# Performance work log

Hardware: AMD Instinct MI355X
Metric: run time of the kernel (lower is better)

Reference implementation:

```python
import jax, jax.numpy as jnp
import numpy as np

N_NODES = 100000
N_EDGES = 1600000
N_FEAT = 128
HIDDEN = 128
N_CLASSES = 10
N_GRAPHS = 512


def setup_inputs() -> dict:
    key = jax.random.key(0)
    ks = jax.random.split(key, 20)

    def lin(k, fan_in, fan_out, bias=True):
        kw, kb = jax.random.split(k)
        s = 1.0 / np.sqrt(fan_in)
        W = jax.random.uniform(kw, (fan_in, fan_out), jnp.float32, -s, s)
        if bias:
            b = jax.random.uniform(kb, (fan_out,), jnp.float32, -s, s)
            return W, b
        return W

    x = jax.random.normal(ks[0], (N_NODES, N_FEAT), jnp.float32)
    edge_index = jax.random.randint(ks[1], (2, N_EDGES), 0, N_NODES)
    batch = jnp.sort(jax.random.randint(ks[2], (N_NODES,), 0, N_GRAPHS))

    w1l, b1 = lin(ks[3], N_FEAT, HIDDEN)
    w1r = lin(ks[4], N_FEAT, HIDDEN, bias=False)
    w2l, b2 = lin(ks[5], HIDDEN, HIDDEN)
    w2r = lin(ks[6], HIDDEN, HIDDEN, bias=False)
    w3l, b3 = lin(ks[7], HIDDEN, HIDDEN)
    w3r = lin(ks[8], HIDDEN, HIDDEN, bias=False)
    gate_w, gate_b = lin(ks[9], HIDDEN, 1)
    lin1_w, lin1_b = lin(ks[10], HIDDEN, HIDDEN)
    lin2_w, lin2_b = lin(ks[11], HIDDEN, N_CLASSES)

    return dict(x=x, edge_index=edge_index, batch=batch,
                w1l=w1l, b1=b1, w1r=w1r,
                w2l=w2l, b2=b2, w2r=w2r,
                w3l=w3l, b3=b3, w3r=w3r,
                gate_w=gate_w, gate_b=gate_b,
                lin1_w=lin1_w, lin1_b=lin1_b,
                lin2_w=lin2_w, lin2_b=lin2_b)


def _sage_conv(x, src, dst, Wl, bl, Wr, n_nodes):
    # PyG SAGEConv(mean): out = lin_l(mean_{j in N(i)} x_j) + lin_r(x_i)
    msg_sum = jax.ops.segment_sum(x[src], dst, num_segments=n_nodes)
    cnt = jax.ops.segment_sum(jnp.ones((src.shape[0], 1), x.dtype), dst,
                              num_segments=n_nodes)
    mean = msg_sum / jnp.maximum(cnt, 1.0)
    return mean @ Wl + bl + x @ Wr


def reference(x, edge_index, batch,
              w1l, b1, w1r, w2l, b2, w2r, w3l, b3, w3r,
              gate_w, gate_b, lin1_w, lin1_b, lin2_w, lin2_b):
    n = x.shape[0]
    src, dst = edge_index[0], edge_index[1]

    h = jax.nn.relu(_sage_conv(x, src, dst, w1l, b1, w1r, n))
    h = jax.nn.relu(_sage_conv(h, src, dst, w2l, b2, w2r, n))
    h = jax.nn.relu(_sage_conv(h, src, dst, w3l, b3, w3r, n))

    # AttentionalAggregation: scatter-softmax of gate over graph segments
    gate = h @ gate_w + gate_b                                  # [N, 1]
    m = jax.ops.segment_max(gate, batch, num_segments=N_GRAPHS)  # [G, 1]
    e = jnp.exp(gate - m[batch])
    s = jax.ops.segment_sum(e, batch, num_segments=N_GRAPHS)     # [G, 1]
    alpha = e / s[batch]
    pooled = jax.ops.segment_sum(alpha * h, batch, num_segments=N_GRAPHS)  # [G, H]

    out = jax.nn.relu(pooled @ lin1_w + lin1_b)
    # dropout is identity in eval mode
    out = out @ lin2_w + lin2_b
    return jax.nn.log_softmax(out, axis=-1)
```

## Files before the change

### kernel.cpp

```cpp
#include <hip/hip_runtime.h>
#include <stdint.h>

#define N_NODES 100000
#define N_EDGES 1600000
#define NF 128
#define NG 512
#define NC 10

#define NBUCK ((N_NODES + 255) / 256)
#define EPB 8192

#define BSTRIDE 264

#define CVT_B 6250
#define BT_B 384
#define BOUNDS_B 3
#define COUNT_B ((N_EDGES + EPB - 1) / EPB)

typedef short short8 __attribute__((ext_vector_type(8)));
typedef float f32x4 __attribute__((ext_vector_type(4)));

__device__ __forceinline__ unsigned short f2b(float f) {
    unsigned u = __float_as_uint(f);
    u += 0x7fffu + ((u >> 16) & 1u);
    return (unsigned short)(u >> 16);
}
__device__ __forceinline__ float lo16(unsigned v) { return __uint_as_float(v << 16); }
__device__ __forceinline__ float hi16(unsigned v) { return __uint_as_float(v & 0xffff0000u); }

__global__ __launch_bounds__(256) void prep_kernel(const float* __restrict__ x, unsigned short* __restrict__ xb,
                                                   const float* __restrict__ w1l, const float* __restrict__ w1r,
                                                   const float* __restrict__ w2l, const float* __restrict__ w2r,
                                                   const float* __restrict__ w3l, const float* __restrict__ w3r,
                                                   unsigned short* __restrict__ Bt,
                                                   const int* __restrict__ batch, int* __restrict__ gstart,
                                                   const int* __restrict__ dst, int* __restrict__ bcount) {
    const int b = blockIdx.x, t = threadIdx.x;
    if (b < CVT_B) {
        int i = b * 256 + t;
        const float4* ip = (const float4*)x;
        float4 a = ip[2 * i], c = ip[2 * i + 1];
        uint4 o;
        o.x = (unsigned)f2b(a.x) | ((unsigned)f2b(a.y) << 16);
        o.y = (unsigned)f2b(a.z) | ((unsigned)f2b(a.w) << 16);
        o.z = (unsigned)f2b(c.x) | ((unsigned)f2b(c.y) << 16);
        o.w = (unsigned)f2b(c.z) | ((unsigned)f2b(c.w) << 16);
        ((uint4*)xb)[i] = o;
    } else if (b < CVT_B + BT_B) {
        int i = (b - CVT_B) * 256 + t;
        int layer = i / (128 * 256);
        int r = i % (128 * 256);
        int n = r / 256, k = r % 256;
        const float* wl = (layer == 0) ? w1l : (layer == 1) ? w2l : w3l;
        const float* wr = (layer == 0) ? w1r : (layer == 1) ? w2r : w3r;
        float v = (k < 128) ? wl[k * 128 + n] : wr[(k - 128) * 128 + n];
        Bt[i] = f2b(v);
    } else if (b < CVT_B + BT_B + BOUNDS_B) {
        int g = (b - CVT_B - BT_B) * 256 + t;
        if (g > NG) return;
        int lo = 0, hi = N_NODES;
        while (lo < hi) {
            int mid = (lo + hi) >> 1;
            if (batch[mid] < g) lo = mid + 1; else hi = mid;
        }
        gstart[g] = lo;
    } else {
        __shared__ int h[NBUCK];
        for (int i = t; i < NBUCK; i += 256) h[i] = 0;
        __syncthreads();
        const int base = (b - CVT_B - BT_B - BOUNDS_B) * EPB;
        const int lim = min(base + EPB, N_EDGES);
        for (int i = base + t; i < lim; i += 256) atomicAdd(&h[dst[i] >> 8], 1);
        __syncthreads();
        for (int i = t; i < NBUCK; i += 256)
            if (h[i]) atomicAdd(&bcount[i], h[i]);
    }
}

__global__ __launch_bounds__(512) void bucket_scan(const int* __restrict__ bcount, int* __restrict__ bbase,
                                                   int* __restrict__ gcursor, int* __restrict__ rowptr) {
    __shared__ int sh[512];
    const int t = threadIdx.x;
    int v = (t < NBUCK) ? bcount[t] : 0;
    sh[t] = v;
    __syncthreads();
    for (int off = 1; off < 512; off <<= 1) {
        int u = (t >= off) ? sh[t - off] : 0;
        __syncthreads();
        sh[t] += u;
        __syncthreads();
    }
    if (t < NBUCK) {
        int e = sh[t] - v;
        bbase[t] = e;
        gcursor[t] = e;
    }
    if (t == NBUCK - 1) bbase[NBUCK] = sh[t];
    if (t == 0) rowptr[N_NODES] = N_EDGES;
}

__global__ __launch_bounds__(256) void bucket_scatter(const int* __restrict__ src, const int* __restrict__ dst,
                                                      int* __restrict__ gcursor, unsigned* __restrict__ brec) {
    __shared__ int h[NBUCK];
    for (int i = threadIdx.x; i < NBUCK; i += 256) h[i] = 0;
    __syncthreads();
    const int base = blockIdx.x * EPB;
    const int lim = min(base + EPB, N_EDGES);
    for (int i = base + threadIdx.x; i < lim; i += 256) atomicAdd(&h[dst[i] >> 8], 1);
    __syncthreads();
    for (int i = threadIdx.x; i < NBUCK; i += 256) {
        int c = h[i];
        if (c) h[i] = atomicAdd(&gcursor[i], c);
    }
    __syncthreads();
    for (int i = base + threadIdx.x; i < lim; i += 256) {
        int d = dst[i];
        int pos = atomicAdd(&h[d >> 8], 1);
        brec[pos] = ((unsigned)(d & 255) << 17) | (unsigned)src[i];
    }
}

__global__ __launch_bounds__(256) void bucket_fill(const unsigned* __restrict__ brec, const int* __restrict__ bbase,
                                                   int* __restrict__ rowptr, int* __restrict__ eidx) {
    __shared__ int nh[256];
    __shared__ int sc[256];
    const int b = blockIdx.x, t = threadIdx.x;
    const int beg = bbase[b], end = bbase[b + 1];
    nh[t] = 0;
    __syncthreads();
    for (int i = beg + t; i < end; i += 256) atomicAdd(&nh[brec[i] >> 17], 1);
    __syncthreads();
    int cnt = nh[t];
    sc[t] = cnt;
    __syncthreads();
    for (int off = 1; off < 256; off <<= 1) {
        int u = (t >= off) ? sc[t - off] : 0;
        __syncthreads();
        sc[t] += u;
        __syncthreads();
    }
    int excl = sc[t] - cnt;
    int node = b * 256 + t;
    if (node < N_NODES) rowptr[node] = beg + excl;
    nh[t] = beg + excl;
    __syncthreads();
    for (int i = beg + t; i < end; i += 256) {
        unsigned r = brec[i];
        int pos = atomicAdd(&nh[r >> 17], 1);
        eidx[pos] = (int)(r & 0x1FFFFu);
    }
}

__global__ __launch_bounds__(256) void agg_kernel(const unsigned short* __restrict__ F,
                                                  const int* __restrict__ rowptr,
                                                  const int* __restrict__ eidx,
                                                  unsigned short* __restrict__ M) {
    int node = blockIdx.x * 4 + (threadIdx.x >> 6);
    if (node >= N_NODES) return;
    const int lane = threadIdx.x & 63;
    const int quad = lane >> 4, ql = lane & 15;
    const int beg = rowptr[node], end = rowptr[node + 1];
    const uint4* F4 = (const uint4*)F;

    float a0 = 0.f, a1 = 0.f, a2 = 0.f, a3 = 0.f, a4 = 0.f, a5 = 0.f, a6 = 0.f, a7 = 0.f;
    int t = beg + quad;
    for (; t + 12 < end; t += 16) {
        int r0 = eidx[t];
        int r1 = eidx[t + 4];
        int r2 = eidx[t + 8];
        int r3 = eidx[t + 12];
        uint4 v0 = F4[(size_t)r0 * 16 + ql];
        uint4 v1 = F4[(size_t)r1 * 16 + ql];
        uint4 v2 = F4[(size_t)r2 * 16 + ql];
        uint4 v3 = F4[(size_t)r3 * 16 + ql];
        a0 += lo16(v0.x) + lo16(v1.x) + lo16(v2.x) + lo16(v3.x);
        a1 += hi16(v0.x) + hi16(v1.x) + hi16(v2.x) + hi16(v3.x);
        a2 += lo16(v0.y) + lo16(v1.y) + lo16(v2.y) + lo16(v3.y);
        a3 += hi16(v0.y) + hi16(v1.y) + hi16(v2.y) + hi16(v3.y);
        a4 += lo16(v0.z) + lo16(v1.z) + lo16(v2.z) + lo16(v3.z);
        a5 += hi16(v0.z) + hi16(v1.z) + hi16(v2.z) + hi16(v3.z);
        a6 += lo16(v0.w) + lo16(v1.w) + lo16(v2.w) + lo16(v3.w);
        a7 += hi16(v0.w) + hi16(v1.w) + hi16(v2.w) + hi16(v3.w);
    }
    for (; t < end; t += 4) {
        uint4 v0 = F4[(size_t)eidx[t] * 16 + ql];
        a0 += lo16(v0.x); a1 += hi16(v0.x);
        a2 += lo16(v0.y); a3 += hi16(v0.y);
        a4 += lo16(v0.z); a5 += hi16(v0.z);
        a6 += lo16(v0.w); a7 += hi16(v0.w);
    }
    a0 += __shfl_xor(a0, 16); a0 += __shfl_xor(a0, 32);
    a1 += __shfl_xor(a1, 16); a1 += __shfl_xor(a1, 32);
    a2 += __shfl_xor(a2, 16); a2 += __shfl_xor(a2, 32);
    a3 += __shfl_xor(a3, 16); a3 += __shfl_xor(a3, 32);
    a4 += __shfl_xor(a4, 16); a4 += __shfl_xor(a4, 32);
    a5 += __shfl_xor(a5, 16); a5 += __shfl_xor(a5, 32);
    a6 += __shfl_xor(a6, 16); a6 += __shfl_xor(a6, 32);
    a7 += __shfl_xor(a7, 16); a7 += __shfl_xor(a7, 32);

    if (quad == 0) {
        float inv = 1.0f / (float)max(end - beg, 1);
        uint4 o;
        o.x = (unsigned)f2b(a0 * inv) | ((unsigned)f2b(a1 * inv) << 16);
        o.y = (unsigned)f2b(a2 * inv) | ((unsigned)f2b(a3 * inv) << 16);
        o.z = (unsigned)f2b(a4 * inv) | ((unsigned)f2b(a5 * inv) << 16);
        o.w = (unsigned)f2b(a6 * inv) | ((unsigned)f2b(a7 * inv) << 16);
        ((uint4*)M)[(size_t)node * 16 + ql] = o;
    }
}

__global__ __launch_bounds__(256, 2) void gemm_kernel(const unsigned short* __restrict__ Am,
                                                      const unsigned short* __restrict__ Ax,
                                                      const unsigned short* __restrict__ Bt,
                                                      const float* __restrict__ bias,
                                                      unsigned short* __restrict__ Out,
                                                      const float* __restrict__ gatew,
                                                      const float* __restrict__ gateb,
                                                      float* __restrict__ gate) {
    const int t = threadIdx.x;
    const int wave = t >> 6, lane = t & 63;
    const int lrow = lane & 15, quad = lane >> 4;
    const int row0 = blockIdx.x * 256 + wave * 64;

    __shared__ __attribute__((aligned(16))) unsigned short Bs[128 * BSTRIDE];

#pragma unroll
    for (int i = 0; i < 16; ++i) {
        int u = t + i * 256;
        int r = u >> 5, seg = u & 31;
        *(uint4*)(Bs + r * BSTRIDE + seg * 8) = *(const uint4*)(Bt + r * 256 + seg * 8);
    }
    __syncthreads();

    f32x4 acc[4][8];
#pragma unroll
    for (int i = 0; i < 4; ++i)
#pragma unroll
        for (int j = 0; j < 8; ++j) acc[i][j] = (f32x4){0.f, 0.f, 0.f, 0.f};

#pragma unroll
    for (int c = 0; c < 8; ++c) {
        const unsigned short* Aarr = (c < 4) ? Am : Ax;
        const int kb = (c & 3) * 32 + quad * 8;
        const int kf = c * 32 + quad * 8;
        short8 af[4];
#pragma unroll
        for (int i = 0; i < 4; ++i) {
            int ar = row0 + i * 16 + lrow;
            if (ar > N_NODES - 1) ar = N_NODES - 1;
            af[i] = *(const short8*)(Aarr + (size_t)ar * 128 + kb);
        }
#pragma unroll
        for (int j = 0; j < 8; ++j) {
            short8 bf = *(const short8*)(Bs + (j * 16 + lrow) * BSTRIDE + kf);
#pragma unroll
            for (int i = 0; i < 4; ++i)
                acc[i][j] = __builtin_amdgcn_mfma_f32_16x16x32_bf16(af[i], bf, acc[i][j], 0, 0, 0);
        }
    }

    float gpart[4][4];
#pragma unroll
    for (int i = 0; i < 4; ++i)
#pragma unroll
        for (int r = 0; r < 4; ++r) gpart[i][r] = 0.f;

#pragma unroll
    for (int j = 0; j < 8; ++j) {
        int col = j * 16 + lrow;
        float bc = bias[col];
        float gw = gatew ? gatew[col] : 0.f;
#pragma unroll
        for (int i = 0; i < 4; ++i) {
            int rbase = row0 + i * 16 + quad * 4;
#pragma unroll
            for (int r = 0; r < 4; ++r) {
                int row = rbase + r;
                if (row < N_NODES) {
                    float v = fmaxf(acc[i][j][r] + bc, 0.f);
                    Out[(size_t)row * 128 + col] = f2b(v);
                    gpart[i][r] += v * gw;
                }
            }
        }
    }
    if (gatew) {
        float gb = gateb[0];
#pragma unroll
        for (int i = 0; i < 4; ++i) {
#pragma unroll
            for (int r = 0; r < 4; ++r) {
                float g = gpart[i][r];
                g += __shfl_xor(g, 1);
                g += __shfl_xor(g, 2);
                g += __shfl_xor(g, 4);
                g += __shfl_xor(g, 8);
                if (lrow == 0) {
                    int row = row0 + i * 16 + quad * 4 + r;
                    if (row < N_NODES) gate[row] = g + gb;
                }
            }
        }
    }
}

__global__ __launch_bounds__(256) void pool_mlp_kernel(const unsigned short* __restrict__ h,
                                                       const float* __restrict__ gate,
                                                       const int* __restrict__ gstart,
                                                       const float* __restrict__ l1w,
                                                       const float* __restrict__ l1b,
                                                       const float* __restrict__ l2w,
                                                       const float* __restrict__ l2b,
                                                       float* __restrict__ out) {
    int wv = threadIdx.x >> 6;
    int g = blockIdx.x * 4 + wv;
    int lane = threadIdx.x & 63;
    __shared__ float pooled_s[4][128];
    __shared__ float hid_s[4][128];
    if (g >= NG) return;

    int beg = gstart[g], end = gstart[g + 1];

    float m = -INFINITY;
    for (int i = beg + lane; i < end; i += 64) m = fmaxf(m, gate[i]);
#pragma unroll
    for (int o = 32; o; o >>= 1) m = fmaxf(m, __shfl_xor(m, o));
    float s = 0.f;
    for (int i = beg + lane; i < end; i += 64) s += expf(gate[i] - m);
#pragma unroll
    for (int o = 32; o; o >>= 1) s += __shfl_xor(s, o);
    float invs = (s > 0.f) ? 1.0f / s : 0.f;

    float ax = 0.f, ay = 0.f;
    const unsigned* hb = (const unsigned*)h;
    int i = beg;
    for (; i + 2 <= end; i += 2) {
        float w0 = expf(gate[i] - m) * invs;
        float w1 = expf(gate[i + 1] - m) * invs;
        unsigned v0 = hb[(size_t)i * 64 + lane];
        unsigned v1 = hb[(size_t)(i + 1) * 64 + lane];
        ax += w0 * lo16(v0) + w1 * lo16(v1);
        ay += w0 * hi16(v0) + w1 * hi16(v1);
    }
    for (; i < end; ++i) {
        float w = expf(gate[i] - m) * invs;
        unsigned v = hb[(size_t)i * 64 + lane];
        ax += w * lo16(v);
        ay += w * hi16(v);
    }
    pooled_s[wv][2 * lane] = ax;
    pooled_s[wv][2 * lane + 1] = ay;

    float h0 = l1b[lane], h1 = l1b[lane + 64];
    for (int k = 0; k < 128; ++k) {
        float pv = pooled_s[wv][k];
        h0 += pv * l1w[k * 128 + lane];
        h1 += pv * l1w[k * 128 + lane + 64];
    }
    hid_s[wv][lane] = fmaxf(h0, 0.f);
    hid_s[wv][lane + 64] = fmaxf(h1, 0.f);

    float o10 = 0.f;
    if (lane < NC) {
        o10 = l2b[lane];
        for (int k = 0; k < 128; ++k) o10 += hid_s[wv][k] * l2w[k * NC + lane];
    }
    float mm = -INFINITY;
#pragma unroll
    for (int j = 0; j < NC; ++j) mm = fmaxf(mm, __shfl(o10, j));
    float ss = 0.f;
#pragma unroll
    for (int j = 0; j < NC; ++j) ss += expf(__shfl(o10, j) - mm);
    float lse = mm + logf(ss);
    if (lane < NC) out[g * NC + lane] = o10 - lse;
}

extern "C" void kernel_launch(void* const* d_in, const int* in_sizes, int n_in,
                              void* d_out, int out_size, void* d_ws, size_t ws_size,
                              hipStream_t stream) {
    const float* x   = (const float*)d_in[0];
    const int* ei    = (const int*)d_in[1];
    const int* batch = (const int*)d_in[2];
    const float* w1l = (const float*)d_in[3];
    const float* b1  = (const float*)d_in[4];
    const float* w1r = (const float*)d_in[5];
    const float* w2l = (const float*)d_in[6];
    const float* b2  = (const float*)d_in[7];
    const float* w2r = (const float*)d_in[8];
    const float* w3l = (const float*)d_in[9];
    const float* b3  = (const float*)d_in[10];
    const float* w3r = (const float*)d_in[11];
    const float* gw  = (const float*)d_in[12];
    const float* gb  = (const float*)d_in[13];
    const float* l1w = (const float*)d_in[14];
    const float* l1b = (const float*)d_in[15];
    const float* l2w = (const float*)d_in[16];
    const float* l2b = (const float*)d_in[17];
    float* out = (float*)d_out;

    const int* src = ei;
    const int* dst = ei + N_EDGES;

    char* base = (char*)d_ws;
    size_t off = 0;
    auto carve = [&](size_t bytes) -> void* {
        void* r = base + off;
        off = (off + bytes + 255) & ~(size_t)255;
        return r;
    };
    int* rowptr         = (int*)carve((size_t)(N_NODES + 1) * 4);
    int* eidx           = (int*)carve((size_t)N_EDGES * 4);
    unsigned short* Bt  = (unsigned short*)carve((size_t)3 * 128 * 256 * 2);
    unsigned short* xb  = (unsigned short*)carve((size_t)N_NODES * NF * 2);
    unsigned short* mn  = (unsigned short*)carve((size_t)N_NODES * NF * 2);
    unsigned short* hA  = (unsigned short*)carve((size_t)N_NODES * NF * 2);
    unsigned short* hB  = (unsigned short*)carve((size_t)N_NODES * NF * 2);
    float* gate         = (float*)carve((size_t)N_NODES * 4);
    int* gstart         = (int*)carve(513 * 4);
    int* bcount         = (int*)carve((NBUCK + 1) * 4);
    int* bbase          = (int*)carve((NBUCK + 1) * 4);
    int* gcursor        = (int*)carve((NBUCK + 1) * 4);
    unsigned* brec      = (unsigned*)mn;

    hipMemsetAsync(bcount, 0, (size_t)NBUCK * 4, stream);

    prep_kernel<<<CVT_B + BT_B + BOUNDS_B + COUNT_B, 256, 0, stream>>>(
        x, xb, w1l, w1r, w2l, w2r, w3l, w3r, Bt, batch, gstart, dst, bcount);

    bucket_scan<<<1, 512, 0, stream>>>(bcount, bbase, gcursor, rowptr);
    bucket_scatter<<<COUNT_B, 256, 0, stream>>>(src, dst, gcursor, brec);
    bucket_fill<<<NBUCK, 256, 0, stream>>>(brec, bbase, rowptr, eidx);

    const int AGG_B = (N_NODES + 3) / 4;
    const int GEMM_B = (N_NODES + 255) / 256;

    agg_kernel<<<AGG_B, 256, 0, stream>>>(xb, rowptr, eidx, mn);
    gemm_kernel<<<GEMM_B, 256, 0, stream>>>(mn, xb, Bt, b1, hA, nullptr, nullptr, nullptr);
    agg_kernel<<<AGG_B, 256, 0, stream>>>(hA, rowptr, eidx, mn);
    gemm_kernel<<<GEMM_B, 256, 0, stream>>>(mn, hA, Bt + 32768, b2, hB, nullptr, nullptr, nullptr);
    agg_kernel<<<AGG_B, 256, 0, stream>>>(hB, rowptr, eidx, mn);
    gemm_kernel<<<GEMM_B, 256, 0, stream>>>(mn, hB, Bt + 65536, b3, hA, gw, gb, gate);

    pool_mlp_kernel<<<(NG + 3) / 4, 256, 0, stream>>>(hA, gate, gstart, l1w, l1b, l2w, l2b, out);
}
```

Baseline: 507.0 us.

## Fuse neighbor-mean aggregation with MFMA GEMM per 64-node tile

Replaces the separate aggregation and GEMM kernels with one kernel per layer. Each block gathers neighbor means for 64 nodes into shared memory, then runs the bf16 MFMA GEMM in two 64-column passes with half-size weight tiles in LDS. This removes the global write and re-read of the mean buffer and three kernel launches. In exchange, each block reloads the weight tiles for only 64 rows and the gather phase is serialized with the GEMM inside a block, which may cut overlap and occupancy.

```diff
diff --git a/kernel.cpp b/kernel.cpp
--- a/kernel.cpp
+++ b/kernel.cpp
@@ -11,6 +11,7 @@
 #define EPB 8192
 
 #define BSTRIDE 264
+#define MSTRIDE 136
 
 #define CVT_B 6250
 #define BT_B 384
@@ -151,154 +152,144 @@
     }
 }
 
-__global__ __launch_bounds__(256) void agg_kernel(const unsigned short* __restrict__ F,
-                                                  const int* __restrict__ rowptr,
-                                                  const int* __restrict__ eidx,
-                                                  unsigned short* __restrict__ M) {
-    int node = blockIdx.x * 4 + (threadIdx.x >> 6);
-    if (node >= N_NODES) return;
-    const int lane = threadIdx.x & 63;
-    const int quad = lane >> 4, ql = lane & 15;
-    const int beg = rowptr[node], end = rowptr[node + 1];
-    const uint4* F4 = (const uint4*)F;
-
-    float a0 = 0.f, a1 = 0.f, a2 = 0.f, a3 = 0.f, a4 = 0.f, a5 = 0.f, a6 = 0.f, a7 = 0.f;
-    int t = beg + quad;
-    for (; t + 12 < end; t += 16) {
-        int r0 = eidx[t];
-        int r1 = eidx[t + 4];
-        int r2 = eidx[t + 8];
-        int r3 = eidx[t + 12];
-        uint4 v0 = F4[(size_t)r0 * 16 + ql];
-        uint4 v1 = F4[(size_t)r1 * 16 + ql];
-        uint4 v2 = F4[(size_t)r2 * 16 + ql];
-        uint4 v3 = F4[(size_t)r3 * 16 + ql];
-        a0 += lo16(v0.x) + lo16(v1.x) + lo16(v2.x) + lo16(v3.x);
-        a1 += hi16(v0.x) + hi16(v1.x) + hi16(v2.x) + hi16(v3.x);
-        a2 += lo16(v0.y) + lo16(v1.y) + lo16(v2.y) + lo16(v3.y);
-        a3 += hi16(v0.y) + hi16(v1.y) + hi16(v2.y) + hi16(v3.y);
-        a4 += lo16(v0.z) + lo16(v1.z) + lo16(v2.z) + lo16(v3.z);
-        a5 += hi16(v0.z) + hi16(v1.z) + hi16(v2.z) + hi16(v3.z);
-        a6 += lo16(v0.w) + lo16(v1.w) + lo16(v2.w) + lo16(v3.w);
-        a7 += hi16(v0.w) + hi16(v1.w) + hi16(v2.w) + hi16(v3.w);
-    }
-    for (; t < end; t += 4) {
-        uint4 v0 = F4[(size_t)eidx[t] * 16 + ql];
-        a0 += lo16(v0.x); a1 += hi16(v0.x);
-        a2 += lo16(v0.y); a3 += hi16(v0.y);
-        a4 += lo16(v0.z); a5 += hi16(v0.z);
-        a6 += lo16(v0.w); a7 += hi16(v0.w);
-    }
-    a0 += __shfl_xor(a0, 16); a0 += __shfl_xor(a0, 32);
-    a1 += __shfl_xor(a1, 16); a1 += __shfl_xor(a1, 32);
-    a2 += __shfl_xor(a2, 16); a2 += __shfl_xor(a2, 32);
-    a3 += __shfl_xor(a3, 16); a3 += __shfl_xor(a3, 32);
-    a4 += __shfl_xor(a4, 16); a4 += __shfl_xor(a4, 32);
-    a5 += __shfl_xor(a5, 16); a5 += __shfl_xor(a5, 32);
-    a6 += __shfl_xor(a6, 16); a6 += __shfl_xor(a6, 32);
-    a7 += __shfl_xor(a7, 16); a7 += __shfl_xor(a7, 32);
-
-    if (quad == 0) {
-        float inv = 1.0f / (float)max(end - beg, 1);
-        uint4 o;
-        o.x = (unsigned)f2b(a0 * inv) | ((unsigned)f2b(a1 * inv) << 16);
-        o.y = (unsigned)f2b(a2 * inv) | ((unsigned)f2b(a3 * inv) << 16);
-        o.z = (unsigned)f2b(a4 * inv) | ((unsigned)f2b(a5 * inv) << 16);
-        o.w = (unsigned)f2b(a6 * inv) | ((unsigned)f2b(a7 * inv) << 16);
-        ((uint4*)M)[(size_t)node * 16 + ql] = o;
-    }
-}
-
-__global__ __launch_bounds__(256, 2) void gemm_kernel(const unsigned short* __restrict__ Am,
-                                                      const unsigned short* __restrict__ Ax,
-                                                      const unsigned short* __restrict__ Bt,
-                                                      const float* __restrict__ bias,
-                                                      unsigned short* __restrict__ Out,
-                                                      const float* __restrict__ gatew,
-                                                      const float* __restrict__ gateb,
-                                                      float* __restrict__ gate) {
+__global__ __launch_bounds__(256) void fused_layer(const unsigned short* __restrict__ F,
+                                                   const int* __restrict__ rowptr,
+                                                   const int* __restrict__ eidx,
+                                                   const unsigned short* __restrict__ Bt,
+                                                   const float* __restrict__ bias,
+                                                   unsigned short* __restrict__ Out,
+                                                   const float* __restrict__ gatew,
+                                                   const float* __restrict__ gateb,
+                                                   float* __restrict__ gate) {
     const int t = threadIdx.x;
     const int wave = t >> 6, lane = t & 63;
     const int lrow = lane & 15, quad = lane >> 4;
-    const int row0 = blockIdx.x * 256 + wave * 64;
-
-    __shared__ __attribute__((aligned(16))) unsigned short Bs[128 * BSTRIDE];
-
-#pragma unroll
-    for (int i = 0; i < 16; ++i) {
-        int u = t + i * 256;
-        int r = u >> 5, seg = u & 31;
-        *(uint4*)(Bs + r * BSTRIDE + seg * 8) = *(const uint4*)(Bt + r * 256 + seg * 8);
-    }
-    __syncthreads();
-
-    f32x4 acc[4][8];
-#pragma unroll
-    for (int i = 0; i < 4; ++i)
-#pragma unroll
-        for (int j = 0; j < 8; ++j) acc[i][j] = (f32x4){0.f, 0.f, 0.f, 0.f};
-
-#pragma unroll
-    for (int c = 0; c < 8; ++c) {
-        const unsigned short* Aarr = (c < 4) ? Am : Ax;
-        const int kb = (c & 3) * 32 + quad * 8;
-        const int kf = c * 32 + quad * 8;
-        short8 af[4];
-#pragma unroll
-        for (int i = 0; i < 4; ++i) {
-            int ar = row0 + i * 16 + lrow;
-            if (ar > N_NODES - 1) ar = N_NODES - 1;
-            af[i] = *(const short8*)(Aarr + (size_t)ar * 128 + kb);
-        }
-#pragma unroll
-        for (int j = 0; j < 8; ++j) {
-            short8 bf = *(const short8*)(Bs + (j * 16 + lrow) * BSTRIDE + kf);
-#pragma unroll
-            for (int i = 0; i < 4; ++i)
-                acc[i][j] = __builtin_amdgcn_mfma_f32_16x16x32_bf16(af[i], bf, acc[i][j], 0, 0, 0);
-        }
-    }
-
-    float gpart[4][4];
-#pragma unroll
-    for (int i = 0; i < 4; ++i)
-#pragma unroll
-        for (int r = 0; r < 4; ++r) gpart[i][r] = 0.f;
-
-#pragma unroll
-    for (int j = 0; j < 8; ++j) {
-        int col = j * 16 + lrow;
-        float bc = bias[col];
-        float gw = gatew ? gatew[col] : 0.f;
-#pragma unroll
-        for (int i = 0; i < 4; ++i) {
-            int rbase = row0 + i * 16 + quad * 4;
+    const int row0 = blockIdx.x * 64;
+
+    __shared__ __attribute__((aligned(16))) unsigned short meanS[64 * MSTRIDE];
+    __shared__ __attribute__((aligned(16))) unsigned short Bs[64 * BSTRIDE];
+
+    const uint4* F4 = (const uint4*)F;
+
+    for (int n = 0; n < 16; ++n) {
+        int node = row0 + wave * 16 + n;
+        if (node >= N_NODES) break;
+        const int beg = rowptr[node], end = rowptr[node + 1];
+        float a0 = 0.f, a1 = 0.f, a2 = 0.f, a3 = 0.f, a4 = 0.f, a5 = 0.f, a6 = 0.f, a7 = 0.f;
+        int e = beg + quad;
+        for (; e + 12 < end; e += 16) {
+            int r0 = eidx[e];
+            int r1 = eidx[e + 4];
+            int r2 = eidx[e + 8];
+            int r3 = eidx[e + 12];
+            uint4 v0 = F4[(size_t)r0 * 16 + lrow];
+            uint4 v1 = F4[(size_t)r1 * 16 + lrow];
+            uint4 v2 = F4[(size_t)r2 * 16 + lrow];
+            uint4 v3 = F4[(size_t)r3 * 16 + lrow];
+            a0 += lo16(v0.x) + lo16(v1.x) + lo16(v2.x) + lo16(v3.x);
+            a1 += hi16(v0.x) + hi16(v1.x) + hi16(v2.x) + hi16(v3.x);
+            a2 += lo16(v0.y) + lo16(v1.y) + lo16(v2.y) + lo16(v3.y);
+            a3 += hi16(v0.y) + hi16(v1.y) + hi16(v2.y) + hi16(v3.y);
+            a4 += lo16(v0.z) + lo16(v1.z) + lo16(v2.z) + lo16(v3.z);
+            a5 += hi16(v0.z) + hi16(v1.z) + hi16(v2.z) + hi16(v3.z);
+            a6 += lo16(v0.w) + lo16(v1.w) + lo16(v2.w) + lo16(v3.w);
+            a7 += hi16(v0.w) + hi16(v1.w) + hi16(v2.w) + hi16(v3.w);
+        }
+        for (; e < end; e += 4) {
+            uint4 v0 = F4[(size_t)eidx[e] * 16 + lrow];
+            a0 += lo16(v0.x); a1 += hi16(v0.x);
+            a2 += lo16(v0.y); a3 += hi16(v0.y);
+            a4 += lo16(v0.z); a5 += hi16(v0.z);
+            a6 += lo16(v0.w); a7 += hi16(v0.w);
+        }
+        a0 += __shfl_xor(a0, 16); a0 += __shfl_xor(a0, 32);
+        a1 += __shfl_xor(a1, 16); a1 += __shfl_xor(a1, 32);
+        a2 += __shfl_xor(a2, 16); a2 += __shfl_xor(a2, 32);
+        a3 += __shfl_xor(a3, 16); a3 += __shfl_xor(a3, 32);
+        a4 += __shfl_xor(a4, 16); a4 += __shfl_xor(a4, 32);
+        a5 += __shfl_xor(a5, 16); a5 += __shfl_xor(a5, 32);
+        a6 += __shfl_xor(a6, 16); a6 += __shfl_xor(a6, 32);
+        a7 += __shfl_xor(a7, 16); a7 += __shfl_xor(a7, 32);
+        if (quad == 0) {
+            float inv = 1.0f / (float)max(end - beg, 1);
+            uint4 o;
+            o.x = (unsigned)f2b(a0 * inv) | ((unsigned)f2b(a1 * inv) << 16);
+            o.y = (unsigned)f2b(a2 * inv) | ((unsigned)f2b(a3 * inv) << 16);
+            o.z = (unsigned)f2b(a4 * inv) | ((unsigned)f2b(a5 * inv) << 16);
+            o.w = (unsigned)f2b(a6 * inv) | ((unsigned)f2b(a7 * inv) << 16);
+            *(uint4*)(meanS + (wave * 16 + n) * MSTRIDE + lrow * 8) = o;
+        }
+    }
+    __syncthreads();
+
+    int arow = row0 + wave * 16 + lrow;
+    if (arow > N_NODES - 1) arow = N_NODES - 1;
+
+    float gpart[4] = {0.f, 0.f, 0.f, 0.f};
+    short8 afg[4];
+
+    for (int pass = 0; pass < 2; ++pass) {
+        if (pass) __syncthreads();
+#pragma unroll
+        for (int i = 0; i < 8; ++i) {
+            int u = t + i * 256;
+            int r = u >> 5, seg = u & 31;
+            *(uint4*)(Bs + r * BSTRIDE + seg * 8) =
+                *(const uint4*)(Bt + (size_t)(pass * 64 + r) * 256 + seg * 8);
+        }
+        __syncthreads();
+
+        f32x4 acc[4];
+#pragma unroll
+        for (int j = 0; j < 4; ++j) acc[j] = (f32x4){0.f, 0.f, 0.f, 0.f};
+
+#pragma unroll
+        for (int c = 0; c < 8; ++c) {
+            short8 af;
+            if (c < 4) {
+                af = *(const short8*)(meanS + (wave * 16 + lrow) * MSTRIDE + c * 32 + quad * 8);
+            } else {
+                if (pass == 0)
+                    afg[c - 4] = *(const short8*)(F + (size_t)arow * 128 + (c - 4) * 32 + quad * 8);
+                af = afg[c - 4];
+            }
+            const int kf = c * 32 + quad * 8;
+#pragma unroll
+            for (int j = 0; j < 4; ++j) {
+                short8 bf = *(const short8*)(Bs + (j * 16 + lrow) * BSTRIDE + kf);
+                acc[j] = __builtin_amdgcn_mfma_f32_16x16x32_bf16(af, bf, acc[j], 0, 0, 0);
+            }
+        }
+
+#pragma unroll
+        for (int j = 0; j < 4; ++j) {
+            int col = pass * 64 + j * 16 + lrow;
+            float bc = bias[col];
+            float gw = gatew ? gatew[col] : 0.f;
 #pragma unroll
             for (int r = 0; r < 4; ++r) {
-                int row = rbase + r;
+                int row = row0 + wave * 16 + quad * 4 + r;
                 if (row < N_NODES) {
-                    float v = fmaxf(acc[i][j][r] + bc, 0.f);
+                    float v = fmaxf(acc[j][r] + bc, 0.f);
                     Out[(size_t)row * 128 + col] = f2b(v);
-                    gpart[i][r] += v * gw;
+                    gpart[r] += v * gw;
                 }
             }
         }
     }
+
     if (gatew) {
         float gb = gateb[0];
 #pragma unroll
-        for (int i = 0; i < 4; ++i) {
-#pragma unroll
-            for (int r = 0; r < 4; ++r) {
-                float g = gpart[i][r];
-                g += __shfl_xor(g, 1);
-                g += __shfl_xor(g, 2);
-                g += __shfl_xor(g, 4);
-                g += __shfl_xor(g, 8);
-                if (lrow == 0) {
-                    int row = row0 + i * 16 + quad * 4 + r;
-                    if (row < N_NODES) gate[row] = g + gb;
-                }
+        for (int r = 0; r < 4; ++r) {
+            float g = gpart[r];
+            g += __shfl_xor(g, 1);
+            g += __shfl_xor(g, 2);
+            g += __shfl_xor(g, 4);
+            g += __shfl_xor(g, 8);
+            if (lrow == 0) {
+                int row = row0 + wave * 16 + quad * 4 + r;
+                if (row < N_NODES) gate[row] = g + gb;
             }
         }
     }
@@ -412,7 +403,6 @@
     int* eidx           = (int*)carve((size_t)N_EDGES * 4);
     unsigned short* Bt  = (unsigned short*)carve((size_t)3 * 128 * 256 * 2);
     unsigned short* xb  = (unsigned short*)carve((size_t)N_NODES * NF * 2);
-    unsigned short* mn  = (unsigned short*)carve((size_t)N_NODES * NF * 2);
     unsigned short* hA  = (unsigned short*)carve((size_t)N_NODES * NF * 2);
     unsigned short* hB  = (unsigned short*)carve((size_t)N_NODES * NF * 2);
     float* gate         = (float*)carve((size_t)N_NODES * 4);
@@ -420,7 +410,7 @@
     int* bcount         = (int*)carve((NBUCK + 1) * 4);
     int* bbase          = (int*)carve((NBUCK + 1) * 4);
     int* gcursor        = (int*)carve((NBUCK + 1) * 4);
-    unsigned* brec      = (unsigned*)mn;
+    unsigned* brec      = (unsigned*)hB;
 
     hipMemsetAsync(bcount, 0, (size_t)NBUCK * 4, stream);
 
@@ -431,15 +421,11 @@
     bucket_scatter<<<COUNT_B, 256, 0, stream>>>(src, dst, gcursor, brec);
     bucket_fill<<<NBUCK, 256, 0, stream>>>(brec, bbase, rowptr, eidx);
 
-    const int AGG_B = (N_NODES + 3) / 4;
-    const int GEMM_B = (N_NODES + 255) / 256;
-
-    agg_kernel<<<AGG_B, 256, 0, stream>>>(xb, rowptr, eidx, mn);
-    gemm_kernel<<<GEMM_B, 256, 0, stream>>>(mn, xb, Bt, b1, hA, nullptr, nullptr, nullptr);
-    agg_kernel<<<AGG_B, 256, 0, stream>>>(hA, rowptr, eidx, mn);
-    gemm_kernel<<<GEMM_B, 256, 0, stream>>>(mn, hA, Bt + 32768, b2, hB, nullptr, nullptr, nullptr);
-    agg_kernel<<<AGG_B, 256, 0, stream>>>(hB, rowptr, eidx, mn);
-    gemm_kernel<<<GEMM_B, 256, 0, stream>>>(mn, hB, Bt + 65536, b3, hA, gw, gb, gate);
+    const int FL_B = (N_NODES + 63) / 64;
+
+    fused_layer<<<FL_B, 256, 0, stream>>>(xb, rowptr, eidx, Bt, b1, hA, nullptr, nullptr, nullptr);
+    fused_layer<<<FL_B, 256, 0, stream>>>(hA, rowptr, eidx, Bt + 32768, b2, hB, nullptr, nullptr, nullptr);
+    fused_layer<<<FL_B, 256, 0, stream>>>(hB, rowptr, eidx, Bt + 65536, b3, hA, gw, gb, gate);
 
     pool_mlp_kernel<<<(NG + 3) / 4, 256, 0, stream>>>(hA, gate, gstart, l1w, l1b, l2w, l2b, out);
 }
```

After: 683.2 us. +34.7%, slower.
